# Optimization experiments

Hardware: AMD Instinct MI355X
Metric: run time of the kernel (lower is better)

The kernel has to match this reference:

```python
import jax, jax.numpy as jnp
import numpy as np

B, S, E, H = 2, 2048, 1024, 16
D = E // H  # head_dim = 64


def setup_inputs() -> dict:
    key = jax.random.key(0)
    ks = jax.random.split(key, 6)
    scale = 1.0 / np.sqrt(E)
    return {
        "x": jax.random.normal(ks[0], (B, S, E), dtype=jnp.float32),
        "Wqkv_w": jax.random.normal(ks[1], (3 * E, E), dtype=jnp.float32) * scale,
        "Wqkv_b": jax.random.normal(ks[2], (3 * E,), dtype=jnp.float32) * 0.01,
        "out_w": jax.random.normal(ks[3], (E, E), dtype=jnp.float32) * scale,
        "out_b": jax.random.normal(ks[4], (E,), dtype=jnp.float32) * 0.01,
        "distance_decay": jax.random.normal(ks[5], (1,), dtype=jnp.float32),
    }


def reference(x, Wqkv_w, Wqkv_b, out_w, out_b, distance_decay):
    b, s, e = x.shape
    # fused QKV projection: (b, s, 3e) -> three (b, h, s, d)
    qkv = x @ Wqkv_w.T + Wqkv_b
    qkv = qkv.reshape(b, s, 3, H, D).transpose(2, 0, 3, 1, 4)  # (3, b, h, s, d)
    q, k, v = qkv[0], qkv[1], qkv[2]
    # scores scaled by 1/sqrt(head_dim)
    scores = jnp.einsum("bhsd,bhtd->bhst", q, k) / jnp.sqrt(jnp.asarray(D, x.dtype))
    # multiplicative exponential distance decay: exp(-|a| * |i-j|)
    idx = jnp.arange(s, dtype=x.dtype)
    dist = jnp.abs(idx[:, None] - idx[None, :])  # (s, s)
    decay = jnp.exp(-jnp.abs(distance_decay[0]) * dist)
    scores = scores * decay  # broadcast over (b, h)
    attn = jax.nn.softmax(scores, axis=-1)
    out = jnp.einsum("bhst,bhtd->bhsd", attn, v)  # (b, h, s, d)
    out = out.transpose(0, 2, 1, 3).reshape(b, s, e)  # (b, s, e)
    return out @ out_w.T + out_b
```

## Files before the change

kernel.cpp:

```cpp
#include <hip/hip_runtime.h>
#include <hip/hip_bf16.h>

#define BN 2
#define SDIM 2048
#define EDIM 1024
#define HN 16
#define DDIM 64

typedef __attribute__((ext_vector_type(8))) short bfrag;
typedef __attribute__((ext_vector_type(4))) float ffrag;

__device__ __forceinline__ ffrag mfma16(bfrag a, bfrag b, ffrag c) {
    return __builtin_amdgcn_mfma_f32_16x16x32_bf16(a, b, c, 0, 0, 0);
}

__device__ __forceinline__ ushort f2bf(float f) {
    union { float f; unsigned u; } un;
    un.f = f;
    unsigned u = un.u;
    u += 0x7fffu + ((u >> 16) & 1u);
    return (ushort)(u >> 16);
}

__device__ __forceinline__ uint pkbf2(float a, float b) {
    __hip_bfloat162 h = __float22bfloat162_rn(make_float2(a, b));
    union { __hip_bfloat162 h; uint u; } cv;
    cv.h = h;
    return cv.u;
}

__device__ __forceinline__ void gld16(const void* g, void* l) {
    __builtin_amdgcn_global_load_lds((const __attribute__((address_space(1))) void*)g,
                                     (__attribute__((address_space(3))) void*)l,
                                     16, 0, 0);
}

__global__ __launch_bounds__(256) void to_bf16_3(const float* __restrict__ a, ushort* __restrict__ oa, int na,
                                                 const float* __restrict__ b, ushort* __restrict__ ob, int nb,
                                                 const float* __restrict__ c, ushort* __restrict__ oc, int nc) {
    int i = (blockIdx.x * 256 + threadIdx.x) * 4;
    const float* src;
    ushort* dst;
    if (i < na)                { src = a + i;            dst = oa + i; }
    else if (i < na + nb)      { src = b + (i - na);     dst = ob + (i - na); }
    else if (i < na + nb + nc) { src = c + (i - na - nb); dst = oc + (i - na - nb); }
    else return;
    float4 v = *(const float4*)src;
    uint2 u;
    u.x = pkbf2(v.x, v.y);
    u.y = pkbf2(v.z, v.w);
    *(uint2*)dst = u;
}

template <int UNUSED>
__global__ __launch_bounds__(512, 4) void gemm192_qkv(const ushort* __restrict__ A,
                                                      const ushort* __restrict__ Bt,
                                                      const float* __restrict__ bias,
                                                      ushort* __restrict__ Cout,
                                                      float* __restrict__ T,
                                                      int M, int N, int K) {
    constexpr int BM = 128, BNT = 192;
    constexpr int A_USH = BM * 64;
    constexpr int B_USH = BNT * 64;
    constexpr int BUF_USH = A_USH + B_USH;
    __shared__ ushort lds[2 * BUF_USH];

    const int tid  = threadIdx.x;
    const int wave = tid >> 6;
    const int lane = tid & 63;
    const int ln16 = lane & 15;
    const int quad = lane >> 4;
    const int wm   = wave >> 2;
    const int wn   = wave & 3;

    const int lid  = blockIdx.y * 32 + blockIdx.x;
    const int xcd  = lid & 7;
    const int rank = lid >> 3;
    const int tx   = (xcd & 3) * 8 + (rank & 7);
    const int ty   = (xcd >> 2) * 8 + (rank >> 3);
    const int bm   = tx * BM;
    const int bn   = ty * BNT;

    const int r0 = tid >> 3;
    const int c0 = ((tid & 7) - r0) & 7;
    const ushort* Abase = A  + (size_t)(bm + r0) * K + c0 * 8;
    const ushort* Bbase = Bt + (size_t)(bn + r0) * K + c0 * 8;
    const int ldst0 = wave * 512;

    const int Ra = wm * 64 + ln16;
    const int Rb = wn * 48 + ln16;
    int aoff[2], boff[2];
#pragma unroll
    for (int kb = 0; kb < 2; ++kb) {
        aoff[kb] = Ra * 64 + ((kb * 4 + quad + Ra) & 7) * 8;
        boff[kb] = A_USH + Rb * 64 + ((kb * 4 + quad + Rb) & 7) * 8;
    }

    ffrag acc[4][3];
#pragma unroll
    for (int mi = 0; mi < 4; ++mi)
#pragma unroll
        for (int ni = 0; ni < 3; ++ni)
            acc[mi][ni] = (ffrag){0.f, 0.f, 0.f, 0.f};

    const int nt = K >> 6;

    auto stA = [&](int buf, int t, int rnd) {
        gld16(Abase + (size_t)rnd * 64 * K + t * 64,
              &lds[buf * BUF_USH + rnd * 4096 + ldst0]);
    };
    auto stB = [&](int buf, int t, int rnd) {
        gld16(Bbase + (size_t)rnd * 64 * K + t * 64,
              &lds[buf * BUF_USH + A_USH + rnd * 4096 + ldst0]);
    };

    stA(0, 0, 0); stA(0, 0, 1);
    stB(0, 0, 0); stB(0, 0, 1); stB(0, 0, 2);
    stB(1, 1, 0); stB(1, 1, 1); stB(1, 1, 2);
    asm volatile("s_waitcnt vmcnt(3)" ::: "memory");
    __builtin_amdgcn_s_barrier();

    for (int t = 0; t < nt; ++t) {
        const int buf = t & 1;
        const ushort* Al = &lds[buf * BUF_USH];
        const bool h1 = (t + 1) < nt;
        const bool h2 = (t + 2) < nt;
        bfrag bfr[3][2];
#pragma unroll
        for (int p = 0; p < 4; ++p) {
            bfrag afr[2];
#pragma unroll
            for (int kb = 0; kb < 2; ++kb)
                afr[kb] = *(const bfrag*)(Al + aoff[kb] + p * 1024);
            if (p == 0) {
#pragma unroll
                for (int ni = 0; ni < 3; ++ni)
#pragma unroll
                    for (int kb = 0; kb < 2; ++kb)
                        bfr[ni][kb] = *(const bfrag*)(Al + boff[kb] + ni * 1024);
            }
            if (p == 0 && h1) stA(buf ^ 1, t + 1, 0);
            if (p == 1 && h1) stA(buf ^ 1, t + 1, 1);
            if (p == 1 && h2) stB(buf, t + 2, 0);
            if (p == 2 && h2) stB(buf, t + 2, 1);
            if (p == 3 && h2) stB(buf, t + 2, 2);

            __builtin_amdgcn_s_barrier();
            asm volatile("s_waitcnt lgkmcnt(0)" ::: "memory");
            __builtin_amdgcn_sched_barrier(0);
            __builtin_amdgcn_s_setprio(1);
#pragma unroll
            for (int ni = 0; ni < 3; ++ni)
#pragma unroll
                for (int kb = 0; kb < 2; ++kb)
                    acc[p][ni] = mfma16(afr[kb], bfr[ni][kb], acc[p][ni]);
            __builtin_amdgcn_s_setprio(0);
            if (p == 3) {
                if (h2)      { asm volatile("s_waitcnt vmcnt(3)" ::: "memory"); }
                else if (h1) { asm volatile("s_waitcnt vmcnt(0)" ::: "memory"); }
            }
            __builtin_amdgcn_s_barrier();
        }
    }

#pragma unroll
    for (int mi = 0; mi < 4; ++mi) {
#pragma unroll
        for (int ni = 0; ni < 3; ++ni) {
            int col = bn + wn * 48 + ni * 16 + ln16;
            float bc = bias[col];
            int row0 = bm + wm * 64 + mi * 16 + quad * 4;
            int which = col >> 10;
            int rem = col & 1023;
            int h = rem >> 6;
            int d = rem & 63;
            int b = row0 >> 11;
            int s0 = row0 & 2047;
            if (which == 2) {
                float v0 = acc[mi][ni][0] + bc, v1 = acc[mi][ni][1] + bc;
                float v2 = acc[mi][ni][2] + bc, v3 = acc[mi][ni][3] + bc;
                uint2 pk;
                pk.x = pkbf2(v0, v1);
                pk.y = pkbf2(v2, v3);
                size_t dst = 2ull * (BN * HN * SDIM * DDIM) +
                             (((size_t)(b * HN + h)) * DDIM + d) * SDIM + s0;
                *(uint2*)(Cout + dst) = pk;
            } else {
                float sc = (which == 0) ? 0.125f : 1.f;
#pragma unroll
                for (int reg = 0; reg < 4; ++reg) {
                    float v = (acc[mi][ni][reg] + bc) * sc;
                    size_t dst = (size_t)which * (BN * HN * SDIM * DDIM) +
                                 (((size_t)(b * HN + h)) * SDIM + s0 + reg) * DDIM + d;
                    Cout[dst] = f2bf(v);
                }
            }
        }
    }

#pragma unroll
    for (int ni = 0; ni < 3; ++ni) {
        int col = bn + wn * 48 + ni * 16 + ln16;
        if ((col >> 10) == 2) {
            float s = 0.f;
#pragma unroll
            for (int mi = 0; mi < 4; ++mi)
#pragma unroll
                for (int reg = 0; reg < 4; ++reg)
                    s += acc[mi][ni][reg];
            s += __shfl_xor(s, 16);
            s += __shfl_xor(s, 32);
            if (quad == 0) {
                float bc = bias[col];
                int rem = col & 1023;
                int h = rem >> 6, d = rem & 63;
                int b = bm >> 11;
                int tile_g = ((bm & 2047) >> 6) + wm;
                T[(((size_t)(b * HN + h)) * 32 + tile_g) * 64 + d] = s + 64.f * bc;
            }
        }
    }
}

__global__ __launch_bounds__(512, 4) void gemm64_op(const ushort* __restrict__ A,
                                                    const ushort* __restrict__ Bt,
                                                    const float* __restrict__ bias,
                                                    float* __restrict__ C,
                                                    int M, int N, int K) {
    constexpr int BM = 64, BNT = 128;
    constexpr int A_USH = BM * 64;
    constexpr int B_USH = BNT * 64;
    constexpr int BUF_USH = A_USH + B_USH;
    __shared__ ushort lds[2 * BUF_USH];

    const int tid  = threadIdx.x;
    const int wave = tid >> 6;
    const int lane = tid & 63;
    const int ln16 = lane & 15;
    const int quad = lane >> 4;
    const int wm   = wave >> 2;
    const int wn   = wave & 3;
    const int bm   = blockIdx.x * BM;
    const int bn   = blockIdx.y * BNT;

    const int r0 = tid >> 3;
    const int c0 = ((tid & 7) - r0) & 7;
    const ushort* Abase = A  + (size_t)(bm + r0) * K + c0 * 8;
    const ushort* Bbase = Bt + (size_t)(bn + r0) * K + c0 * 8;
    const int ldst0 = wave * 512;

    const int Ra = wm * 32 + ln16;
    const int Rb = wn * 32 + ln16;
    int aoff[2], boff[2];
#pragma unroll
    for (int kb = 0; kb < 2; ++kb) {
        aoff[kb] = Ra * 64 + ((kb * 4 + quad + Ra) & 7) * 8;
        boff[kb] = A_USH + Rb * 64 + ((kb * 4 + quad + Rb) & 7) * 8;
    }

    ffrag acc[2][2];
#pragma unroll
    for (int mi = 0; mi < 2; ++mi)
#pragma unroll
        for (int ni = 0; ni < 2; ++ni)
            acc[mi][ni] = (ffrag){0.f, 0.f, 0.f, 0.f};

    const int nt = K >> 6;

    auto stA = [&](int buf, int t) {
        gld16(Abase + t * 64, &lds[buf * BUF_USH + ldst0]);
    };
    auto stB = [&](int buf, int t, int rnd) {
        gld16(Bbase + (size_t)rnd * 64 * K + t * 64,
              &lds[buf * BUF_USH + A_USH + rnd * 4096 + ldst0]);
    };

    stA(0, 0); stB(0, 0, 0); stB(0, 0, 1);
    stA(1, 1); stB(1, 1, 0); stB(1, 1, 1);
    asm volatile("s_waitcnt vmcnt(3)" ::: "memory");
    __builtin_amdgcn_s_barrier();

    for (int t = 0; t < nt; ++t) {
        const int buf = t & 1;
        const ushort* Al = &lds[buf * BUF_USH];
        bfrag afr[2][2], bfr[2][2];
#pragma unroll
        for (int mi = 0; mi < 2; ++mi)
#pragma unroll
            for (int kb = 0; kb < 2; ++kb)
                afr[mi][kb] = *(const bfrag*)(Al + aoff[kb] + mi * 1024);
#pragma unroll
        for (int ni = 0; ni < 2; ++ni)
#pragma unroll
            for (int kb = 0; kb < 2; ++kb)
                bfr[ni][kb] = *(const bfrag*)(Al + boff[kb] + ni * 1024);
        asm volatile("s_waitcnt lgkmcnt(0)" ::: "memory");
        __builtin_amdgcn_sched_barrier(0);
        __builtin_amdgcn_s_barrier();

        if (t + 2 < nt) {
            stA(buf, t + 2); stB(buf, t + 2, 0); stB(buf, t + 2, 1);
        }

        __builtin_amdgcn_s_setprio(1);
#pragma unroll
        for (int mi = 0; mi < 2; ++mi)
#pragma unroll
            for (int ni = 0; ni < 2; ++ni)
#pragma unroll
                for (int kb = 0; kb < 2; ++kb)
                    acc[mi][ni] = mfma16(afr[mi][kb], bfr[ni][kb], acc[mi][ni]);
        __builtin_amdgcn_s_setprio(0);

        if (t + 2 < nt)      { asm volatile("s_waitcnt vmcnt(3)" ::: "memory"); }
        else if (t + 1 < nt) { asm volatile("s_waitcnt vmcnt(0)" ::: "memory"); }
        __builtin_amdgcn_s_barrier();
    }

#pragma unroll
    for (int mi = 0; mi < 2; ++mi) {
#pragma unroll
        for (int ni = 0; ni < 2; ++ni) {
            int col = bn + wn * 32 + ni * 16 + ln16;
            float bc = bias[col];
            int row0 = bm + wm * 32 + mi * 16 + quad * 4;
#pragma unroll
            for (int reg = 0; reg < 4; ++reg)
                C[(size_t)(row0 + reg) * N + col] = acc[mi][ni][reg] + bc;
        }
    }
}

__global__ __launch_bounds__(512, 4) void flash_attn(const ushort* __restrict__ Qb,
                                                     const ushort* __restrict__ Kb,
                                                     const ushort* __restrict__ Vtb,
                                                     const float* __restrict__ decay_ptr,
                                                     const float* __restrict__ T,
                                                     ushort* __restrict__ Ob) {
    __shared__ ushort KVs[2][2][4096];
    __shared__ ushort Pb[128][72];
    __shared__ float  Fv[64];

    const int tid  = threadIdx.x;
    const int wave = tid >> 6;
    const int lane = tid & 63;
    const int ln16 = lane & 15;
    const int quad = lane >> 4;

    const int bh = blockIdx.y;
    const int q0 = blockIdx.x * 128;
    const size_t head_off = (size_t)bh * SDIM * DDIM;
    const float absa = fabsf(decay_ptr[0]);
    const float LOG2E = 1.442695041f;
    const float M0L2 = -17.3123404f;
    const float E12 = 6.144212353e-6f;

    int Dstar = (absa > 1e-5f) ? (int)ceilf(16.0f / absa) : (4 * SDIM);
    int lo = q0 - 63 - Dstar; if (lo < 0) lo = 0;
    int hi = q0 + 127 + Dstar; if (hi > SDIM - 1) hi = SDIM - 1;
    const int tlo = lo >> 6;
    const int thi = hi >> 6;
    const int ntiles = thi - tlo + 1;

    if (tid < 64) {
        const float* Tp = T + (size_t)bh * 32 * 64;
        float s = 0.f;
        for (int k = 0; k < tlo; ++k)      s += Tp[k * 64 + tid];
        for (int k = thi + 1; k < 32; ++k) s += Tp[k * 64 + tid];
        Fv[tid] = s;
    }

    auto stageKV = [&](int t0, int buf) {
        int g0 = wave * 64;
        int g  = g0 + lane;
        int r  = g >> 3;
        int c  = (g - r) & 7;
        gld16(Kb  + head_off + (size_t)(t0 + r) * DDIM + c * 8,
              (ushort*)&KVs[buf][0][0] + g0 * 8);
        gld16(Vtb + head_off + (size_t)r * SDIM + t0 + c * 8,
              (ushort*)&KVs[buf][1][0] + g0 * 8);
    };

#pragma unroll
    for (int p = 0; p < 2; ++p) {
        int idx = p * 512 + tid;
        int r = idx >> 3, c = (idx & 7) * 8;
        *(uint4*)&Pb[r][c] = *(const uint4*)(Qb + head_off + (size_t)(q0 + r) * DDIM + c);
    }
    stageKV(tlo * 64, 0);
    __syncthreads();

    bfrag aq[2];
#pragma unroll
    for (int kb = 0; kb < 2; ++kb)
        aq[kb] = *(const bfrag*)&Pb[wave * 16 + ln16][kb * 32 + quad * 8];

    bfrag ones;
#pragma unroll
    for (int i = 0; i < 8; ++i) ones[i] = (short)0x3F80;

    float EcB[4], FcB[4], Epw[4], Fpw[4];
#pragma unroll
    for (int reg = 0; reg < 4; ++reg) {
        int cr = quad * 4 + reg;
        EcB[reg] = __expf(-absa * (float)(15 - cr));
        FcB[reg] = __expf(-absa * (float)cr);
    }
#pragma unroll
    for (int ni = 0; ni < 4; ++ni) {
        Epw[ni] = __expf(-absa * (float)(16 * (3 - ni)));
        Fpw[ni] = __expf(-absa * (float)(16 * ni));
    }
    const float Er = __expf(-absa * (float)ln16);
    const float Fr = __expf(-absa * (float)(15 - ln16));

    ffrag lacc = (ffrag){0.f, 0.f, 0.f, 0.f};
    ffrag o[4];
#pragma unroll
    for (int ni = 0; ni < 4; ++ni) o[ni] = (ffrag){0.f, 0.f, 0.f, 0.f};

    const int m = wave * 16 + ln16;

    for (int it = 0; it < ntiles; ++it) {
        const int t0 = (tlo + it) * 64;
        const int buf = it & 1;
        if (it + 1 < ntiles) stageKV(t0 + 64, buf ^ 1);

        const ushort* Kt = &KVs[buf][0][0];
        const ushort* Vt = &KVs[buf][1][0];

        ffrag sc[4];
#pragma unroll
        for (int ni = 0; ni < 4; ++ni) {
            ffrag a = (ffrag){0.f, 0.f, 0.f, 0.f};
            const int rk = ni * 16 + ln16;
#pragma unroll
            for (int kb = 0; kb < 2; ++kb) {
                bfrag kf = *(const bfrag*)&Kt[rk * 64 + ((kb * 4 + quad + rk) & 7) * 8];
                a = mfma16(kf, aq[kb], a);
            }
            sc[ni] = a;
        }

        const int ds = q0 + wave * 16 - t0;
        float hh = 0.f;
        if (ds >= 64)       hh = __expf(-absa * (float)(ds - 63)) * Er * LOG2E;
        else if (ds <= -16) hh = __expf(-absa * (float)(-ds - 15)) * Fr * LOG2E;

#pragma unroll
        for (int ni = 0; ni < 4; ++ni) {
            float f0, f1, f2, f3;
            if (ds >= 64) {
                float hn = hh * Epw[ni];
                f0 = hn * EcB[0]; f1 = hn * EcB[1]; f2 = hn * EcB[2]; f3 = hn * EcB[3];
            } else if (ds <= -16) {
                float hn = hh * Fpw[ni];
                f0 = hn * FcB[0]; f1 = hn * FcB[1]; f2 = hn * FcB[2]; f3 = hn * FcB[3];
            } else {
                int c0 = ni * 16 + quad * 4;
                f0 = __expf(-absa * fabsf((float)(ds + ln16 - c0)))     * LOG2E;
                f1 = __expf(-absa * fabsf((float)(ds + ln16 - c0 - 1))) * LOG2E;
                f2 = __expf(-absa * fabsf((float)(ds + ln16 - c0 - 2))) * LOG2E;
                f3 = __expf(-absa * fabsf((float)(ds + ln16 - c0 - 3))) * LOG2E;
            }
            float p0 = exp2f(fmaf(sc[ni][0], f0, M0L2));
            float p1 = exp2f(fmaf(sc[ni][1], f1, M0L2));
            float p2 = exp2f(fmaf(sc[ni][2], f2, M0L2));
            float p3 = exp2f(fmaf(sc[ni][3], f3, M0L2));
            uint2 pk;
            pk.x = pkbf2(p0, p1);
            pk.y = pkbf2(p2, p3);
            *(uint2*)&Pb[m][ni * 16 + quad * 4] = pk;
        }

        bfrag ap[2];
#pragma unroll
        for (int kb = 0; kb < 2; ++kb)
            ap[kb] = *(const bfrag*)&Pb[m][kb * 32 + quad * 8];

#pragma unroll
        for (int kb = 0; kb < 2; ++kb)
            lacc = mfma16(ones, ap[kb], lacc);
#pragma unroll
        for (int ni = 0; ni < 4; ++ni) {
            const int rv = ni * 16 + ln16;
#pragma unroll
            for (int kb = 0; kb < 2; ++kb) {
                bfrag vf = *(const bfrag*)&Vt[rv * 64 + ((kb * 4 + quad + rv) & 7) * 8];
                o[ni] = mfma16(vf, ap[kb], o[ni]);
            }
        }
        __syncthreads();
    }

    const float farl = E12 * (float)(SDIM - 64 * ntiles);
    const float inv = 1.f / (lacc[0] + farl);
    const int b = bh / HN, h = bh % HN;
    const int s = q0 + m;
    ushort* dst = Ob + ((size_t)(b * SDIM + s)) * EDIM + h * DDIM + quad * 4;
#pragma unroll
    for (int ni = 0; ni < 4; ++ni) {
        int d0 = ni * 16 + quad * 4;
        float v0 = (o[ni][0] + E12 * Fv[d0 + 0]) * inv;
        float v1 = (o[ni][1] + E12 * Fv[d0 + 1]) * inv;
        float v2 = (o[ni][2] + E12 * Fv[d0 + 2]) * inv;
        float v3 = (o[ni][3] + E12 * Fv[d0 + 3]) * inv;
        uint2 pk;
        pk.x = pkbf2(v0, v1);
        pk.y = pkbf2(v2, v3);
        *(uint2*)(dst + ni * 16) = pk;
    }
}

extern "C" void kernel_launch(void* const* d_in, const int* in_sizes, int n_in,
                              void* d_out, int out_size, void* d_ws, size_t ws_size,
                              hipStream_t stream) {
    const float* x      = (const float*)d_in[0];
    const float* Wqkv_w = (const float*)d_in[1];
    const float* Wqkv_b = (const float*)d_in[2];
    const float* out_w  = (const float*)d_in[3];
    const float* out_b  = (const float*)d_in[4];
    const float* dd     = (const float*)d_in[5];

    char* ws = (char*)d_ws;
    const size_t MB = 1024 * 1024;
    ushort* xb    = (ushort*)(ws + 0 * MB);
    ushort* wqkvb = (ushort*)(ws + 8 * MB);
    ushort* owb   = (ushort*)(ws + 14 * MB);
    ushort* qkvb  = (ushort*)(ws + 16 * MB);
    ushort* ob    = (ushort*)(ws + 40 * MB);
    float*  Tp    = (float*)(ws + 48 * MB);

    const int n_x = BN * SDIM * EDIM;
    const int n_w = 3 * EDIM * EDIM;
    const int n_o = EDIM * EDIM;
    const int HSD = BN * HN * SDIM * DDIM;

    to_bf16_3<<<(n_x + n_w + n_o) / 1024, 256, 0, stream>>>(
        x, xb, n_x, Wqkv_w, wqkvb, n_w, out_w, owb, n_o);

    gemm192_qkv<0><<<dim3(32, 16), 512, 0, stream>>>(xb, wqkvb, Wqkv_b, qkvb, Tp,
                                                     BN * SDIM, 3 * EDIM, EDIM);

    flash_attn<<<dim3(SDIM / 128, BN * HN), 512, 0, stream>>>(
        qkvb, qkvb + HSD, qkvb + 2 * HSD, dd, Tp, ob);

    gemm64_op<<<dim3(64, 8), 512, 0, stream>>>(ob, owb, out_b, (float*)d_out,
                                               BN * SDIM, EDIM, EDIM);
}
```

Measured before the change: 157.5 us.

## Cut QKV GEMM main-loop barriers by batching LDS fragment loads into two phases

Restructures the bf16 QKV-projection GEMM inner loop. The four per-row-block phases, each with two workgroup barriers, become two half-tile compute phases with one mid-tile barrier and one end barrier. All B fragments and the first two A fragments are loaded up front, and the global-to-LDS prefetch issues are grouped around the single mid-tile barrier. The aim is to cut barrier and waitcnt stalls and give the MFMA stream longer uninterrupted runs. The cost is higher register pressure from holding more fragments at once, and the prefetch work is now spread less evenly across the loop.

```diff
diff --git a/kernel.cpp b/kernel.cpp
--- a/kernel.cpp
+++ b/kernel.cpp
@@ -125,42 +125,57 @@
         const ushort* Al = &lds[buf * BUF_USH];
         const bool h1 = (t + 1) < nt;
         const bool h2 = (t + 2) < nt;
-        bfrag bfr[3][2];
-#pragma unroll
-        for (int p = 0; p < 4; ++p) {
-            bfrag afr[2];
+
+        bfrag bfr[3][2], afr01[2][2];
+#pragma unroll
+        for (int ni = 0; ni < 3; ++ni)
 #pragma unroll
             for (int kb = 0; kb < 2; ++kb)
-                afr[kb] = *(const bfrag*)(Al + aoff[kb] + p * 1024);
-            if (p == 0) {
-#pragma unroll
-                for (int ni = 0; ni < 3; ++ni)
-#pragma unroll
-                    for (int kb = 0; kb < 2; ++kb)
-                        bfr[ni][kb] = *(const bfrag*)(Al + boff[kb] + ni * 1024);
-            }
-            if (p == 0 && h1) stA(buf ^ 1, t + 1, 0);
-            if (p == 1 && h1) stA(buf ^ 1, t + 1, 1);
-            if (p == 1 && h2) stB(buf, t + 2, 0);
-            if (p == 2 && h2) stB(buf, t + 2, 1);
-            if (p == 3 && h2) stB(buf, t + 2, 2);
-
-            __builtin_amdgcn_s_barrier();
-            asm volatile("s_waitcnt lgkmcnt(0)" ::: "memory");
-            __builtin_amdgcn_sched_barrier(0);
-            __builtin_amdgcn_s_setprio(1);
+                bfr[ni][kb] = *(const bfrag*)(Al + boff[kb] + ni * 1024);
+#pragma unroll
+        for (int mi = 0; mi < 2; ++mi)
+#pragma unroll
+            for (int kb = 0; kb < 2; ++kb)
+                afr01[mi][kb] = *(const bfrag*)(Al + aoff[kb] + mi * 1024);
+        if (h1) { stA(buf ^ 1, t + 1, 0); stA(buf ^ 1, t + 1, 1); }
+
+        asm volatile("s_waitcnt lgkmcnt(0)" ::: "memory");
+        __builtin_amdgcn_sched_barrier(0);
+        __builtin_amdgcn_s_barrier();
+
+        if (h2) { stB(buf, t + 2, 0); stB(buf, t + 2, 1); stB(buf, t + 2, 2); }
+
+        __builtin_amdgcn_s_setprio(1);
+#pragma unroll
+        for (int mi = 0; mi < 2; ++mi)
 #pragma unroll
             for (int ni = 0; ni < 3; ++ni)
 #pragma unroll
                 for (int kb = 0; kb < 2; ++kb)
-                    acc[p][ni] = mfma16(afr[kb], bfr[ni][kb], acc[p][ni]);
-            __builtin_amdgcn_s_setprio(0);
-            if (p == 3) {
-                if (h2)      { asm volatile("s_waitcnt vmcnt(3)" ::: "memory"); }
-                else if (h1) { asm volatile("s_waitcnt vmcnt(0)" ::: "memory"); }
-            }
-            __builtin_amdgcn_s_barrier();
-        }
+                    acc[mi][ni] = mfma16(afr01[mi][kb], bfr[ni][kb], acc[mi][ni]);
+        __builtin_amdgcn_s_setprio(0);
+
+        bfrag afr23[2][2];
+#pragma unroll
+        for (int mi = 0; mi < 2; ++mi)
+#pragma unroll
+            for (int kb = 0; kb < 2; ++kb)
+                afr23[mi][kb] = *(const bfrag*)(Al + aoff[kb] + (2 + mi) * 1024);
+        asm volatile("s_waitcnt lgkmcnt(0)" ::: "memory");
+        __builtin_amdgcn_sched_barrier(0);
+        __builtin_amdgcn_s_setprio(1);
+#pragma unroll
+        for (int mi = 0; mi < 2; ++mi)
+#pragma unroll
+            for (int ni = 0; ni < 3; ++ni)
+#pragma unroll
+                for (int kb = 0; kb < 2; ++kb)
+                    acc[2 + mi][ni] = mfma16(afr23[mi][kb], bfr[ni][kb], acc[2 + mi][ni]);
+        __builtin_amdgcn_s_setprio(0);
+
+        if (h2)      { asm volatile("s_waitcnt vmcnt(3)" ::: "memory"); }
+        else if (h1) { asm volatile("s_waitcnt vmcnt(0)" ::: "memory"); }
+        __builtin_amdgcn_s_barrier();
     }
 
 #pragma unroll
```

Result: no change. 157.4 us (-0.1%).
